# Kernel tuning notes

Measured on AMD Instinct MI355X. Metric: run time of the kernel, lower is better.

The kernel has to match this reference:

```python
import jax, jax.numpy as jnp
import numpy as np

MARGIN = 0.5
EPS = 1e-5
NEG_TOPK = 10  # cfg.XBM.NEG_TOPK; memory path (B != M) uses top-k negatives


def setup_inputs() -> dict:
    key = jax.random.key(0)
    k1, k2, k3, k4 = jax.random.split(key, 4)
    B, M, D, C = 256, 65536, 512, 1000
    inputs_col = jax.random.normal(k1, (B, D), dtype=jnp.float32)
    inputs_row = jax.random.normal(k2, (M, D), dtype=jnp.float32)
    targets_col = jax.random.randint(k3, (B,), 0, C)
    target_row = jax.random.randint(k4, (M,), 0, C)
    return {
        "inputs_col": inputs_col,
        "targets_col": targets_col,
        "inputs_row": inputs_row,
        "target_row": target_row,
    }


def reference(inputs_col, targets_col, inputs_row, target_row):
    # sim_mat: [B, M] dense similarity
    sim = jnp.matmul(inputs_col, inputs_row.T)
    same = targets_col[:, None] == target_row[None, :]  # [B, M]

    # positive pairs: same label and sim < 1 - eps; loss = sum(1 - sim)
    pos_mask = same & (sim < 1.0 - EPS)
    pos_loss = jnp.sum(jnp.where(pos_mask, 1.0 - sim, 0.0), axis=1)  # [B]

    # negative pairs (B != M memory path): top-k largest similarities among
    # different-label entries; loss = sum of those top-k values.
    neg_vals = jnp.where(same, -jnp.inf, sim)  # [B, M]
    topk_vals, _ = jax.lax.top_k(neg_vals, NEG_TOPK)  # [B, k]
    neg_loss = jnp.sum(jnp.where(jnp.isfinite(topk_vals), topk_vals, 0.0), axis=1)

    # loss = sum_i (pos_loss_i + neg_loss_i) / n
    return jnp.mean(pos_loss + neg_loss)
```

## Files before the change

kernel.cpp:

```cpp
#include <hip/hip_runtime.h>
#include <math.h>
#include <float.h>

typedef __attribute__((ext_vector_type(4))) float f32x4;
typedef __attribute__((ext_vector_type(8))) __bf16 bf16x8;
typedef __attribute__((ext_vector_type(4))) __bf16 bf16x4;

#define NEG_TOPK 10
#define BROW 256
#define MT 128
#define BK 64
#define SIMSTR 136

__device__ __forceinline__ void topk_ins(float (&top)[NEG_TOPK], float v) {
    #pragma unroll
    for (int q = NEG_TOPK - 1; q >= 1; --q)
        top[q] = fmaxf(fminf(v, top[q - 1]), top[q]);
    top[0] = fmaxf(top[0], v);
}

__device__ __forceinline__ bf16x4 cvt4(float4 v) {
    bf16x4 r;
    r[0] = (__bf16)v.x; r[1] = (__bf16)v.y;
    r[2] = (__bf16)v.z; r[3] = (__bf16)v.w;
    return r;
}

__global__ __launch_bounds__(512, 2) void cl_pass1(
    const float* __restrict__ A,
    const float* __restrict__ Bm,
    const int* __restrict__ tcol,
    const int* __restrict__ trow,
    float* __restrict__ part_topk,
    float* __restrict__ pos_part,
    int D)
{
    __shared__ unsigned short simsb[BROW * SIMSTR];
    __shared__ int trs[MT];
    char* Ab = (char*)simsb;
    char* Bb = Ab + BROW * BK * 2;

    const int mb = blockIdx.x;
    const int j0 = mb * MT;
    const int t  = threadIdx.x;
    const int wave = t >> 6, lane = t & 63;
    const int wr = wave >> 1, wc = wave & 1;
    const int lrow = lane & 15, lk = lane >> 4;

    if (t < MT) trs[t] = trow[j0 + t];

    const float4* A4 = (const float4*)A;
    const float4* B4 = (const float4*)Bm;
    const int ldq = D >> 2;

    f32x4 acc[4][4];
    #pragma unroll
    for (int m = 0; m < 4; ++m)
        #pragma unroll
        for (int n = 0; n < 4; ++n)
            acc[m][n] = (f32x4){0.f, 0.f, 0.f, 0.f};

    float4 ar[8];
    float4 br[4];
    #pragma unroll
    for (int s = 0; s < 8; ++s) {
        int f = s * 512 + t; int r = f >> 4, k4 = f & 15;
        ar[s] = A4[r * ldq + k4];
    }
    #pragma unroll
    for (int s = 0; s < 4; ++s) {
        int f = s * 512 + t; int r = f >> 4, k4 = f & 15;
        br[s] = B4[(size_t)(j0 + r) * ldq + k4];
    }

    const int NSTEP = D / BK;
    for (int step = 0; step < NSTEP; ++step) {
        #pragma unroll
        for (int s = 0; s < 8; ++s) {
            int f = s * 512 + t; int r = f >> 4, k4 = f & 15;
            int off = r * 128 + ((k4 * 8) ^ ((r & 7) << 4));
            *(bf16x4*)(Ab + off) = cvt4(ar[s]);
        }
        #pragma unroll
        for (int s = 0; s < 4; ++s) {
            int f = s * 512 + t; int r = f >> 4, k4 = f & 15;
            int off = r * 128 + ((k4 * 8) ^ ((r & 7) << 4));
            *(bf16x4*)(Bb + off) = cvt4(br[s]);
        }
        __syncthreads();

        if (step + 1 < NSTEP) {
            int kq = (step + 1) * (BK / 4);
            #pragma unroll
            for (int s = 0; s < 8; ++s) {
                int f = s * 512 + t; int r = f >> 4, k4 = f & 15;
                ar[s] = A4[r * ldq + kq + k4];
            }
            #pragma unroll
            for (int s = 0; s < 4; ++s) {
                int f = s * 512 + t; int r = f >> 4, k4 = f & 15;
                br[s] = B4[(size_t)(j0 + r) * ldq + kq + k4];
            }
        }

        const int swz = (lrow & 7) << 4;
        #pragma unroll
        for (int ks = 0; ks < 2; ++ks) {
            bf16x8 af[4], bfr[4];
            const int kb = ks * 64 + lk * 16;
            #pragma unroll
            for (int m = 0; m < 4; ++m) {
                int row = wr * 64 + m * 16 + lrow;
                af[m] = *(const bf16x8*)(Ab + row * 128 + (kb ^ swz));
            }
            #pragma unroll
            for (int n = 0; n < 4; ++n) {
                int row = wc * 64 + n * 16 + lrow;
                bfr[n] = *(const bf16x8*)(Bb + row * 128 + (kb ^ swz));
            }
            #pragma unroll
            for (int m = 0; m < 4; ++m)
                #pragma unroll
                for (int n = 0; n < 4; ++n)
                    acc[m][n] = __builtin_amdgcn_mfma_f32_16x16x32_bf16(
                        af[m], bfr[n], acc[m][n], 0, 0, 0);
        }
        __syncthreads();
    }

    #pragma unroll
    for (int m = 0; m < 4; ++m)
        #pragma unroll
        for (int n = 0; n < 4; ++n)
            #pragma unroll
            for (int r = 0; r < 4; ++r) {
                int row = wr * 64 + m * 16 + lk * 4 + r;
                int col = wc * 64 + n * 16 + lrow;
                __bf16 b = (__bf16)acc[m][n][r];
                simsb[row * SIMSTR + col] = *(unsigned short*)&b;
            }
    __syncthreads();

    {
        const int row = t >> 1, half = t & 1;
        const int myc = tcol[row];
        float top[NEG_TOPK];
        #pragma unroll
        for (int q = 0; q < NEG_TOPK; ++q) top[q] = -INFINITY;
        float pos = 0.f;
        const char* srow = (const char*)simsb + (row * SIMSTR + half * 64) * 2;
        #pragma unroll
        for (int j = 0; j < 8; ++j) {
            bf16x8 v8 = *(const bf16x8*)(srow + j * 16);
            #pragma unroll
            for (int e = 0; e < 8; ++e) {
                float s = (float)v8[e];
                bool same = (trs[half * 64 + j * 8 + e] == myc);
                pos += (same && s < 0.99999f) ? (1.f - s) : 0.f;
                topk_ins(top, same ? -INFINITY : s);
            }
        }
        const int ch = mb * 2 + half;
        float* dst = part_topk + ((size_t)row * 1024 + ch) * NEG_TOPK;
        #pragma unroll
        for (int q = 0; q < NEG_TOPK; ++q) dst[q] = top[q];
        pos_part[(size_t)row * 1024 + ch] = pos;
    }
}

__global__ __launch_bounds__(256) void cl_pass2(
    const float* __restrict__ part_topk,
    const float* __restrict__ pos_part,
    float* __restrict__ row_tot,
    int nch)
{
    const int i = blockIdx.x;
    const int t = threadIdx.x;
    __shared__ float stop[256][NEG_TOPK];
    __shared__ float stop2[32][NEG_TOPK];
    __shared__ float red[256];

    const int n = nch * NEG_TOPK;
    const float* src = part_topk + (size_t)i * n;
    float top[NEG_TOPK];
    #pragma unroll
    for (int q = 0; q < NEG_TOPK; ++q) top[q] = -INFINITY;
    for (int idx = t; idx < n; idx += 256) topk_ins(top, src[idx]);
    #pragma unroll
    for (int q = 0; q < NEG_TOPK; ++q) stop[t][q] = top[q];

    float pos = 0.0f;
    const float* psrc = pos_part + (size_t)i * nch;
    for (int idx = t; idx < nch; idx += 256) pos += psrc[idx];
    red[t] = pos;
    __syncthreads();

    for (int s2 = 128; s2 >= 1; s2 >>= 1) {
        if (t < s2) red[t] += red[t + s2];
        __syncthreads();
    }

    if (t < 32) {
        float m[NEG_TOPK];
        #pragma unroll
        for (int q = 0; q < NEG_TOPK; ++q) m[q] = -INFINITY;
        for (int l = 0; l < 8; ++l)
            #pragma unroll
            for (int q = 0; q < NEG_TOPK; ++q) topk_ins(m, stop[t * 8 + l][q]);
        #pragma unroll
        for (int q = 0; q < NEG_TOPK; ++q) stop2[t][q] = m[q];
    }
    __syncthreads();

    if (t == 0) {
        float m[NEG_TOPK];
        #pragma unroll
        for (int q = 0; q < NEG_TOPK; ++q) m[q] = -INFINITY;
        for (int l = 0; l < 32; ++l)
            #pragma unroll
            for (int q = 0; q < NEG_TOPK; ++q) topk_ins(m, stop2[l][q]);
        float neg = 0.0f;
        #pragma unroll
        for (int q = 0; q < NEG_TOPK; ++q)
            if (isfinite(m[q])) neg += m[q];
        row_tot[i] = neg + red[0];
    }
}

__global__ __launch_bounds__(256) void cl_pass3(
    const float* __restrict__ row_tot, float* __restrict__ out, int Bn)
{
    __shared__ float red[256];
    const int t = threadIdx.x;
    float v = 0.0f;
    for (int idx = t; idx < Bn; idx += 256) v += row_tot[idx];
    red[t] = v;
    __syncthreads();
    for (int s2 = 128; s2 >= 1; s2 >>= 1) {
        if (t < s2) red[t] += red[t + s2];
        __syncthreads();
    }
    if (t == 0) out[0] = red[0] / (float)Bn;
}

extern "C" void kernel_launch(void* const* d_in, const int* in_sizes, int n_in,
                              void* d_out, int out_size, void* d_ws, size_t ws_size,
                              hipStream_t stream)
{
    const float* A    = (const float*)d_in[0];
    const int*   tcol = (const int*)d_in[1];
    const float* Bm   = (const float*)d_in[2];
    const int*   trow = (const int*)d_in[3];
    float* out = (float*)d_out;

    const int Bn = in_sizes[1];
    const int M  = in_sizes[3];
    const int D  = in_sizes[0] / Bn;
    const int numMB = M / MT;
    const int nch = numMB * 2;

    float* part_topk = (float*)d_ws;
    float* pos_part  = part_topk + (size_t)Bn * nch * NEG_TOPK;
    float* row_tot   = pos_part + (size_t)Bn * nch;

    cl_pass1<<<numMB, 512, 0, stream>>>(A, Bm, tcol, trow, part_topk, pos_part, D);
    cl_pass2<<<Bn, 256, 0, stream>>>(part_topk, pos_part, row_tot, nch);
    cl_pass3<<<1, 256, 0, stream>>>(row_tot, out, Bn);
}
```

Baseline: 256.6 us.

## Halve M tile, double-buffer LDS, merge half-row top-k in block

The column tile shrinks from 128 to 64 rows of inputs_row, so there are twice as many blocks, each holding a smaller accumulator set. The single LDS staging buffer becomes a double buffer, so the next K-slice is written while the current one feeds MFMA, which removes one barrier per step. Labels are now read straight from global memory instead of staged in LDS. The two half-row top-k lists are merged inside the block, so each block writes one partial per row. The smaller tile lowers MFMA reuse per byte of A loaded, since A is reloaded by twice as many blocks, and LDS use per block goes up to 80KB.

```diff
diff --git a/kernel.cpp b/kernel.cpp
--- a/kernel.cpp
+++ b/kernel.cpp
@@ -8,9 +8,10 @@
 
 #define NEG_TOPK 10
 #define BROW 256
-#define MT 128
+#define MT 64
 #define BK 64
-#define SIMSTR 136
+#define SIMSTR 72
+#define BUF 40960
 
 __device__ __forceinline__ void topk_ins(float (&top)[NEG_TOPK], float v) {
     #pragma unroll
@@ -35,10 +36,7 @@
     float* __restrict__ pos_part,
     int D)
 {
-    __shared__ unsigned short simsb[BROW * SIMSTR];
-    __shared__ int trs[MT];
-    char* Ab = (char*)simsb;
-    char* Bb = Ab + BROW * BK * 2;
+    __shared__ char smem[2 * BUF];
 
     const int mb = blockIdx.x;
     const int j0 = mb * MT;
@@ -47,95 +45,110 @@
     const int wr = wave >> 1, wc = wave & 1;
     const int lrow = lane & 15, lk = lane >> 4;
 
-    if (t < MT) trs[t] = trow[j0 + t];
-
     const float4* A4 = (const float4*)A;
     const float4* B4 = (const float4*)Bm;
     const int ldq = D >> 2;
-
-    f32x4 acc[4][4];
+    const int NSTEP = D / BK;
+
+    const int ra = t >> 4;
+    const int k4 = t & 15;
+    const int rb = t >> 4;
+
+    f32x4 acc[4][2];
     #pragma unroll
     for (int m = 0; m < 4; ++m)
         #pragma unroll
-        for (int n = 0; n < 4; ++n)
+        for (int n = 0; n < 2; ++n)
             acc[m][n] = (f32x4){0.f, 0.f, 0.f, 0.f};
 
     float4 ar[8];
-    float4 br[4];
-    #pragma unroll
-    for (int s = 0; s < 8; ++s) {
-        int f = s * 512 + t; int r = f >> 4, k4 = f & 15;
-        ar[s] = A4[r * ldq + k4];
-    }
-    #pragma unroll
-    for (int s = 0; s < 4; ++s) {
-        int f = s * 512 + t; int r = f >> 4, k4 = f & 15;
-        br[s] = B4[(size_t)(j0 + r) * ldq + k4];
-    }
-
-    const int NSTEP = D / BK;
+    float4 br[2];
+
+    #pragma unroll
+    for (int s = 0; s < 8; ++s) ar[s] = A4[(ra + 32 * s) * ldq + k4];
+    #pragma unroll
+    for (int s = 0; s < 2; ++s) br[s] = B4[(size_t)(j0 + rb + 32 * s) * ldq + k4];
+    {
+        char* Ab = smem;
+        char* Bb = smem + 32768;
+        #pragma unroll
+        for (int s = 0; s < 8; ++s) {
+            int r = ra + 32 * s;
+            *(bf16x4*)(Ab + r * 128 + ((k4 * 8) ^ ((r & 7) << 4))) = cvt4(ar[s]);
+        }
+        #pragma unroll
+        for (int s = 0; s < 2; ++s) {
+            int r = rb + 32 * s;
+            *(bf16x4*)(Bb + r * 128 + ((k4 * 8) ^ ((r & 7) << 4))) = cvt4(br[s]);
+        }
+    }
+
+    const int swz = (lrow & 7) << 4;
+
     for (int step = 0; step < NSTEP; ++step) {
-        #pragma unroll
-        for (int s = 0; s < 8; ++s) {
-            int f = s * 512 + t; int r = f >> 4, k4 = f & 15;
-            int off = r * 128 + ((k4 * 8) ^ ((r & 7) << 4));
-            *(bf16x4*)(Ab + off) = cvt4(ar[s]);
-        }
-        #pragma unroll
-        for (int s = 0; s < 4; ++s) {
-            int f = s * 512 + t; int r = f >> 4, k4 = f & 15;
-            int off = r * 128 + ((k4 * 8) ^ ((r & 7) << 4));
-            *(bf16x4*)(Bb + off) = cvt4(br[s]);
-        }
+        const int cur = step & 1;
         __syncthreads();
 
         if (step + 1 < NSTEP) {
-            int kq = (step + 1) * (BK / 4);
+            const int kq = (step + 1) * (BK / 4);
+            #pragma unroll
+            for (int s = 0; s < 8; ++s) ar[s] = A4[(ra + 32 * s) * ldq + kq + k4];
+            #pragma unroll
+            for (int s = 0; s < 2; ++s)
+                br[s] = B4[(size_t)(j0 + rb + 32 * s) * ldq + kq + k4];
+        }
+
+        {
+            const char* Ab = smem + cur * BUF;
+            const char* Bb = Ab + 32768;
+            #pragma unroll
+            for (int ks = 0; ks < 2; ++ks) {
+                bf16x8 af[4], bfr[2];
+                const int kb = ks * 64 + lk * 16;
+                #pragma unroll
+                for (int m = 0; m < 4; ++m) {
+                    int row = wr * 64 + m * 16 + lrow;
+                    af[m] = *(const bf16x8*)(Ab + row * 128 + (kb ^ swz));
+                }
+                #pragma unroll
+                for (int n = 0; n < 2; ++n) {
+                    int row = wc * 32 + n * 16 + lrow;
+                    bfr[n] = *(const bf16x8*)(Bb + row * 128 + (kb ^ swz));
+                }
+                #pragma unroll
+                for (int m = 0; m < 4; ++m)
+                    #pragma unroll
+                    for (int n = 0; n < 2; ++n)
+                        acc[m][n] = __builtin_amdgcn_mfma_f32_16x16x32_bf16(
+                            af[m], bfr[n], acc[m][n], 0, 0, 0);
+            }
+        }
+
+        if (step + 1 < NSTEP) {
+            char* Ab = smem + (cur ^ 1) * BUF;
+            char* Bb = Ab + 32768;
             #pragma unroll
             for (int s = 0; s < 8; ++s) {
-                int f = s * 512 + t; int r = f >> 4, k4 = f & 15;
-                ar[s] = A4[r * ldq + kq + k4];
-            }
-            #pragma unroll
-            for (int s = 0; s < 4; ++s) {
-                int f = s * 512 + t; int r = f >> 4, k4 = f & 15;
-                br[s] = B4[(size_t)(j0 + r) * ldq + kq + k4];
-            }
-        }
-
-        const int swz = (lrow & 7) << 4;
-        #pragma unroll
-        for (int ks = 0; ks < 2; ++ks) {
-            bf16x8 af[4], bfr[4];
-            const int kb = ks * 64 + lk * 16;
-            #pragma unroll
-            for (int m = 0; m < 4; ++m) {
-                int row = wr * 64 + m * 16 + lrow;
-                af[m] = *(const bf16x8*)(Ab + row * 128 + (kb ^ swz));
-            }
-            #pragma unroll
-            for (int n = 0; n < 4; ++n) {
-                int row = wc * 64 + n * 16 + lrow;
-                bfr[n] = *(const bf16x8*)(Bb + row * 128 + (kb ^ swz));
-            }
-            #pragma unroll
-            for (int m = 0; m < 4; ++m)
-                #pragma unroll
-                for (int n = 0; n < 4; ++n)
-                    acc[m][n] = __builtin_amdgcn_mfma_f32_16x16x32_bf16(
-                        af[m], bfr[n], acc[m][n], 0, 0, 0);
-        }
-        __syncthreads();
-    }
-
+                int r = ra + 32 * s;
+                *(bf16x4*)(Ab + r * 128 + ((k4 * 8) ^ ((r & 7) << 4))) = cvt4(ar[s]);
+            }
+            #pragma unroll
+            for (int s = 0; s < 2; ++s) {
+                int r = rb + 32 * s;
+                *(bf16x4*)(Bb + r * 128 + ((k4 * 8) ^ ((r & 7) << 4))) = cvt4(br[s]);
+            }
+        }
+    }
+
+    unsigned short* simsb = (unsigned short*)smem;
     #pragma unroll
     for (int m = 0; m < 4; ++m)
         #pragma unroll
-        for (int n = 0; n < 4; ++n)
+        for (int n = 0; n < 2; ++n)
             #pragma unroll
             for (int r = 0; r < 4; ++r) {
                 int row = wr * 64 + m * 16 + lk * 4 + r;
-                int col = wc * 64 + n * 16 + lrow;
+                int col = wc * 32 + n * 16 + lrow;
                 __bf16 b = (__bf16)acc[m][n][r];
                 simsb[row * SIMSTR + col] = *(unsigned short*)&b;
             }
@@ -144,27 +157,40 @@
     {
         const int row = t >> 1, half = t & 1;
         const int myc = tcol[row];
+        const int4* lab4 = (const int4*)(trow + j0 + half * 32);
         float top[NEG_TOPK];
         #pragma unroll
         for (int q = 0; q < NEG_TOPK; ++q) top[q] = -INFINITY;
         float pos = 0.f;
-        const char* srow = (const char*)simsb + (row * SIMSTR + half * 64) * 2;
-        #pragma unroll
-        for (int j = 0; j < 8; ++j) {
-            bf16x8 v8 = *(const bf16x8*)(srow + j * 16);
+        #pragma unroll
+        for (int j = 0; j < 4; ++j) {
+            bf16x8 v8 = *(const bf16x8*)(&simsb[row * SIMSTR + half * 32 + j * 8]);
+            int4 l1 = lab4[2 * j], l2 = lab4[2 * j + 1];
+            int lab[8] = {l1.x, l1.y, l1.z, l1.w, l2.x, l2.y, l2.z, l2.w};
             #pragma unroll
             for (int e = 0; e < 8; ++e) {
                 float s = (float)v8[e];
-                bool same = (trs[half * 64 + j * 8 + e] == myc);
+                bool same = (lab[e] == myc);
                 pos += (same && s < 0.99999f) ? (1.f - s) : 0.f;
                 topk_ins(top, same ? -INFINITY : s);
             }
         }
-        const int ch = mb * 2 + half;
-        float* dst = part_topk + ((size_t)row * 1024 + ch) * NEG_TOPK;
-        #pragma unroll
-        for (int q = 0; q < NEG_TOPK; ++q) dst[q] = top[q];
-        pos_part[(size_t)row * 1024 + ch] = pos;
+        float* mtop = (float*)(smem + BUF);
+        float* mpos = (float*)(smem + BUF + 20480);
+        #pragma unroll
+        for (int q = 0; q < NEG_TOPK; ++q) mtop[t * NEG_TOPK + q] = top[q];
+        mpos[t] = pos;
+        __syncthreads();
+        if (half == 0) {
+            const float* ot = &mtop[(t + 1) * NEG_TOPK];
+            #pragma unroll
+            for (int q = 0; q < NEG_TOPK; ++q) topk_ins(top, ot[q]);
+            float post = pos + mpos[t + 1];
+            float* dst = part_topk + ((size_t)row * gridDim.x + mb) * NEG_TOPK;
+            #pragma unroll
+            for (int q = 0; q < NEG_TOPK; ++q) dst[q] = top[q];
+            pos_part[(size_t)row * gridDim.x + mb] = post;
+        }
     }
 }
 
@@ -257,7 +283,7 @@
     const int M  = in_sizes[3];
     const int D  = in_sizes[0] / Bn;
     const int numMB = M / MT;
-    const int nch = numMB * 2;
+    const int nch = numMB;
 
     float* part_topk = (float*)d_ws;
     float* pos_part  = part_topk + (size_t)Bn * nch * NEG_TOPK;
```

New measurement: 260.2 us. No clear change (+1.4%).
